# Performance work log

Hardware: AMD Instinct MI355X
Metric: run time of the kernel (lower is better)

Reference implementation:

```python
import jax, jax.numpy as jnp
import numpy as np

V = 23
EDGES = [(2,1),(3,1),(6,12),(6,10),(6,8),(8,10),(7,13),(7,11),(7,9),(9,11),(2,4),(4,6),(3,5),(5,7),(2,3),(2,14),(3,15),(14,15),(14,16),(15,17),(16,18),(17,19),(18,20),(18,22),(20,22),(19,21),(19,23),(21,23)]
K, H, C, OUT_C = 3, 8, 128, 128
N, T = 32, 256
BN_EPS = 1e-5


def _hop_matrix():
    # binarized union of I, Fw, Bw as in Graph.get_hop_distance
    A = np.zeros((V, V))
    for i, j in EDGES:
        A[i - 1, j - 1] = 1.0
        A[j - 1, i - 1] = 1.0
    np.fill_diagonal(A, 1.0)
    hop = np.full((V, V), V, dtype=np.int32)
    P = np.eye(V)
    for d in range(V):
        reach = P > 0
        hop = np.where(reach & (hop == V), d, hop)  # smallest d with reachability
        P = P @ A
    assert hop.max() < V, 'graph must be connected'
    return hop


def setup_inputs() -> dict:
    key = jax.random.key(0)
    ks = jax.random.split(key, 8)
    hop = _hop_matrix()  # (V,V) int32, max hop = 8 for mediapipe layout
    n_hop = int(hop.max()) + 1
    cin_g = C // H            # 16 in-channels per group
    cout_g = OUT_C // H       # 16 out-channels per group
    return {
        'x': jax.random.normal(ks[0], (N, C, T, V), dtype=jnp.float32),
        'emb_table': jax.random.normal(ks[1], (K, H, n_hop), dtype=jnp.float32) * 0.1,
        'A': jnp.tile(jnp.eye(V, dtype=jnp.float32)[None, None], (K, H, 1, 1))
             + 0.01 * jax.random.normal(ks[2], (K, H, V, V), dtype=jnp.float32),
        'conv_w': jax.random.normal(ks[3], (K * OUT_C, cin_g), dtype=jnp.float32) * 0.05,
        'conv_b': jax.random.normal(ks[4], (K * OUT_C,), dtype=jnp.float32) * 0.05,
        'bn_gamma': jax.random.uniform(ks[5], (OUT_C,), dtype=jnp.float32, minval=0.5, maxval=1.5),
        'bn_beta': jax.random.normal(ks[6], (OUT_C,), dtype=jnp.float32) * 0.1,
        'bn_mean': jax.random.normal(ks[7], (OUT_C,), dtype=jnp.float32) * 0.1,
        'bn_var': jax.random.uniform(jax.random.fold_in(key, 99), (OUT_C,), dtype=jnp.float32, minval=0.5, maxval=1.5),
        'hop': jnp.asarray(hop),
    }


def reference(x, emb_table, A, conv_w, conv_b, bn_gamma, bn_beta, bn_mean, bn_var, hop):
    n, c, t, v = x.shape
    k, h = A.shape[0], A.shape[1]
    cin_g = c // h
    # per-kernel/per-head learned adjacency from hop embedding table
    B = emb_table[:, :, hop]                                   # (k,h,v,v)
    def l2(w):
        return jnp.sqrt(jnp.sum(w * w, axis=-2, keepdims=True)) + 1e-4
    BnA = B / l2(B) + A / l2(A)                                # (k,h,v,v)
    xh = x.reshape(n, h, cin_g, t, v)
    # graph mixing over nodes (k-dim broadcast of x)
    y = jnp.einsum('nhctv,khvw->nkhctw', xh, BnA)              # (n,k,h,c/h,t,v)
    # grouped 1x1 conv (groups = k*h): per (k,h) group 16->16 channel mix
    w = conv_w.reshape(k, h, -1, cin_g)                        # (k,h,out/h,c/h)
    b = conv_b.reshape(k, h, -1)                               # (k,h,out/h)
    y = jnp.einsum('nkhctv,khoc->nkhotv', y, w) + b[None, :, :, :, None, None]
    y = y.reshape(n, k, -1, t, v).sum(axis=1)                  # (n,out_c,t,v)
    # BatchNorm2d (eval mode)
    inv = bn_gamma / jnp.sqrt(bn_var + BN_EPS)
    y = y * inv[None, :, None, None] + (bn_beta - bn_mean * inv)[None, :, None, None]
    # residual is identity (in_channels == out_channels)
    return jax.nn.relu(y + x)
```

## Files before the change

### kernel.cpp

```cpp
#include <hip/hip_runtime.h>
#include <hip/hip_bf16.h>
#include <stdint.h>

#define V 23
#define VP 24
#define KK 3
#define H 8
#define CG 16
#define TDIM 256
#define NB 32
#define TT 64
#define OUTC 128
#define CIN 128
#define KDIM 384
#define NSTEP 12
#define NCT 24
#define XROW 392

#define WS_BNA   0
#define WS_SCALE (KK*H*VP*VP)
#define WS_OFFS  (WS_SCALE + OUTC)
#define WS_WT    (WS_OFFS + OUTC)
#define WS_MB    (WS_WT + KK*H*CG*CG)
#define MB_ELEMS ((size_t)H * NSTEP * NCT * 512)
#define WS_NEED_BYTES ((size_t)WS_MB * 4 + MB_ELEMS * 2)
#define WS_SMALL_BYTES ((size_t)WS_MB * 4)

typedef __attribute__((ext_vector_type(8))) short bf16x8;
typedef __attribute__((ext_vector_type(4))) float f32x4;

static __device__ __forceinline__ uint32_t f2bf_rne(float f) {
  uint32_t u = __float_as_uint(f);
  return (u + 0x7fffu + ((u >> 16) & 1u)) >> 16;
}
static __device__ __forceinline__ float bf2f(uint16_t h) {
  return __uint_as_float(((uint32_t)h) << 16);
}

__global__ void prep1_kernel(const float* __restrict__ emb,
                             const float* __restrict__ A,
                             const float* __restrict__ conv_w,
                             const float* __restrict__ conv_b,
                             const float* __restrict__ gamma,
                             const float* __restrict__ beta,
                             const float* __restrict__ mean,
                             const float* __restrict__ var,
                             const int* __restrict__ hop,
                             int n_hop, float* __restrict__ ws) {
  int b = blockIdx.x;
  int tid = threadIdx.x;
  if (b < KK * H) {
    int w = tid;
    if (w >= 32) return;
    const float* e = emb + b * n_hop;
    const float* a = A + b * V * V;
    float nb = 1.f, na = 1.f;
    if (w < V) {
      float sb = 0.f, sa = 0.f;
      for (int v = 0; v < V; ++v) {
        float bv = e[hop[v * V + w]];
        float av = a[v * V + w];
        sb += bv * bv;
        sa += av * av;
      }
      nb = sqrtf(sb) + 1e-4f;
      na = sqrtf(sa) + 1e-4f;
    }
    float* dst = ws + WS_BNA + b * VP * VP;
    if (w < VP) {
      for (int v = 0; v < VP; ++v) {
        float val = 0.f;
        if (v < V && w < V)
          val = e[hop[v * V + w]] / nb + a[v * V + w] / na;
        dst[v * VP + w] = val;
      }
    }
  } else if (b == KK * H) {
    if (tid < OUTC) {
      float inv = gamma[tid] * rsqrtf(var[tid] + 1e-5f);
      float sb = conv_b[tid] + conv_b[OUTC + tid] + conv_b[2 * OUTC + tid];
      ws[WS_SCALE + tid] = inv;
      ws[WS_OFFS + tid] = beta[tid] - mean[tid] * inv + sb * inv;
    }
  } else {
    int idx = (b - KK * H - 1) * 256 + tid;
    if (idx < KK * H * CG * CG) {
      int o = idx & 15, c = (idx >> 4) & 15, h = (idx >> 8) & 7, k = idx >> 11;
      ws[WS_WT + ((k * H + h) * CG + c) * CG + o] =
          conv_w[((k * OUTC) + h * CG + o) * CG + c];
    }
  }
}

__global__ void prep2_kernel(float* __restrict__ ws) {
  int b = blockIdx.x;
  int h = b / NSTEP, s = b % NSTEP;
  uint16_t* mb = (uint16_t*)(ws + WS_MB);
  const float* wt = ws + WS_WT;
  const float* bna = ws + WS_BNA;
  for (int e = threadIdx.x; e < NCT * 64 * 8; e += 256) {
    int j = e & 7, lane = (e >> 3) & 63, ct = e >> 9;
    int k = s * 32 + ((lane >> 4) << 3) + j;
    int ci = k / VP, v = k % VP;
    int col = ct * 16 + (lane & 15);
    int o = col / VP, w = col - o * VP;
    float val = 0.f;
    if (v < V && w < V) {
      for (int kk = 0; kk < KK; ++kk)
        val += wt[((kk * H + h) * CG + ci) * CG + o] *
               bna[((kk * H + h) * VP + v) * VP + w];
    }
    mb[((size_t)(h * NSTEP + s) * NCT + ct) * 512 + lane * 8 + j] =
        (uint16_t)f2bf_rne(val);
  }
}

__global__ __launch_bounds__(256, 3) void gcn_main_mfma(
    const float* __restrict__ x,
    const float* __restrict__ ws,
    float* __restrict__ out) {
  __shared__ __align__(16) uint16_t Xa[TT * XROW];

  const int tid = threadIdx.x;
  const int t0 = blockIdx.x * TT;
  const int h  = blockIdx.y;
  const int n  = blockIdx.z;

  for (int u = tid; u < CG * TT * 6; u += 256) {
    int c = u / (TT * 6);
    int r = u % (TT * 6);
    int tt = r / 6, vc = r % 6;
    const float* xrow =
        x + ((size_t)((n * CIN + h * CG + c) * TDIM) + (t0 + tt)) * V;
    float f0 = xrow[vc * 4 + 0];
    float f1 = xrow[vc * 4 + 1];
    float f2 = xrow[vc * 4 + 2];
    float f3 = (vc < 5) ? xrow[vc * 4 + 3] : 0.f;
    uint32_t lo = f2bf_rne(f0) | (f2bf_rne(f1) << 16);
    uint32_t hi = f2bf_rne(f2) | (f2bf_rne(f3) << 16);
    *(uint2*)&Xa[tt * XROW + c * VP + vc * 4] = make_uint2(lo, hi);
  }
  __syncthreads();

  const int wave = tid >> 6, lane = tid & 63;
  const int m = lane & 15, q = lane >> 4;

  const uint16_t* mb = (const uint16_t*)(ws + WS_MB) +
                       ((size_t)h * NSTEP * NCT + wave * 6) * 512 + lane * 8;

  f32x4 acc[4][6];
#pragma unroll
  for (int rt = 0; rt < 4; ++rt)
#pragma unroll
    for (int c6 = 0; c6 < 6; ++c6) acc[rt][c6] = (f32x4){0.f, 0.f, 0.f, 0.f};

  for (int s = 0; s < NSTEP; ++s) {
    bf16x8 bf[6];
#pragma unroll
    for (int c6 = 0; c6 < 6; ++c6)
      bf[c6] = *(const bf16x8*)(mb + (size_t)(s * NCT + c6) * 512);
    bf16x8 af[4];
#pragma unroll
    for (int rt = 0; rt < 4; ++rt)
      af[rt] = *(const bf16x8*)&Xa[(rt * 16 + m) * XROW + s * 32 + q * 8];
#pragma unroll
    for (int c6 = 0; c6 < 6; ++c6)
#pragma unroll
      for (int rt = 0; rt < 4; ++rt)
        acc[rt][c6] = __builtin_amdgcn_mfma_f32_16x16x32_bf16(
            af[rt], bf[c6], acc[rt][c6], 0, 0, 0);
  }

#pragma unroll
  for (int c6 = 0; c6 < 6; ++c6) {
    int col = (wave * 6 + c6) * 16 + m;
    int o = col / VP, w = col - o * VP;
    float sc = ws[WS_SCALE + h * CG + o];
    float of = ws[WS_OFFS + h * CG + o];
    bool valid = (w < V);
    float* obase =
        out + ((size_t)(n * OUTC + h * CG + o) * TDIM + t0) * V + w;
#pragma unroll
    for (int rt = 0; rt < 4; ++rt) {
#pragma unroll
      for (int reg = 0; reg < 4; ++reg) {
        int row = rt * 16 + q * 4 + reg;
        float resid = bf2f(Xa[row * XROW + col]);
        float y = fmaf(acc[rt][c6][reg], sc, of) + resid;
        if (valid) obase[(size_t)row * V] = fmaxf(y, 0.f);
      }
    }
  }
}

__global__ __launch_bounds__(256, 3) void gcn_main_valu(
    const float* __restrict__ x,
    const float* __restrict__ ws,
    float* __restrict__ out) {
  __shared__ __align__(16) uint16_t Xs[CG * TT * VP];

  const int tid = threadIdx.x;
  const int t0 = blockIdx.x * TT;
  const int h  = blockIdx.y;
  const int n  = blockIdx.z;

  for (int u = tid; u < CG * TT * 6; u += 256) {
    int c = u / (TT * 6);
    int r = u % (TT * 6);
    int tt = r / 6, vc = r % 6;
    const float* xrow =
        x + ((size_t)((n * CIN + h * CG + c) * TDIM) + (t0 + tt)) * V;
    float f0 = xrow[vc * 4 + 0];
    float f1 = xrow[vc * 4 + 1];
    float f2 = xrow[vc * 4 + 2];
    float f3 = (vc < 5) ? xrow[vc * 4 + 3] : 0.f;
    uint32_t lo = f2bf_rne(f0) | (f2bf_rne(f1) << 16);
    uint32_t hi = f2bf_rne(f2) | (f2bf_rne(f3) << 16);
    *(uint2*)&Xs[(c * TT + tt) * VP + vc * 4] = make_uint2(lo, hi);
  }
  __syncthreads();

  const int oq = __builtin_amdgcn_readfirstlane(tid >> 6);
  const int tt = tid & 63;

  const float* wt  = ws + WS_WT  + ((size_t)h * CG * CG);
  const float* bna = ws + WS_BNA + ((size_t)h * VP * VP);

  float acc[4][VP];
#pragma unroll
  for (int o = 0; o < 4; ++o)
#pragma unroll
    for (int w = 0; w < VP; ++w) acc[o][w] = 0.f;

  for (int k = 0; k < KK; ++k) {
    const float* wtk  = wt  + (size_t)k * H * CG * CG;
    const float* bnak = bna + (size_t)k * H * VP * VP;
    for (int vb = 0; vb < 3; ++vb) {
      float xwv[4][8];
#pragma unroll
      for (int o = 0; o < 4; ++o)
#pragma unroll
        for (int j = 0; j < 8; ++j) xwv[o][j] = 0.f;
#pragma unroll 4
      for (int c = 0; c < CG; ++c) {
        uint4 raw = *(const uint4*)&Xs[(c * TT + tt) * VP + vb * 8];
        float4 wv = *(const float4*)&wtk[c * CG + (oq << 2)];
        float xv[8];
        xv[0] = __uint_as_float(raw.x << 16);
        xv[1] = __uint_as_float(raw.x & 0xffff0000u);
        xv[2] = __uint_as_float(raw.y << 16);
        xv[3] = __uint_as_float(raw.y & 0xffff0000u);
        xv[4] = __uint_as_float(raw.z << 16);
        xv[5] = __uint_as_float(raw.z & 0xffff0000u);
        xv[6] = __uint_as_float(raw.w << 16);
        xv[7] = __uint_as_float(raw.w & 0xffff0000u);
#pragma unroll
        for (int o = 0; o < 4; ++o) {
          float wo = (&wv.x)[o];
#pragma unroll
          for (int j = 0; j < 8; ++j) xwv[o][j] = fmaf(wo, xv[j], xwv[o][j]);
        }
      }
#pragma unroll
      for (int j = 0; j < 8; ++j) {
        const int v = vb * 8 + j;
        const float* bnrow = &bnak[v * VP];
#pragma unroll
        for (int wb = 0; wb < 6; ++wb) {
          float4 bn = *(const float4*)(bnrow + wb * 4);
#pragma unroll
          for (int o = 0; o < 4; ++o) {
            acc[o][wb * 4 + 0] = fmaf(xwv[o][j], bn.x, acc[o][wb * 4 + 0]);
            acc[o][wb * 4 + 1] = fmaf(xwv[o][j], bn.y, acc[o][wb * 4 + 1]);
            acc[o][wb * 4 + 2] = fmaf(xwv[o][j], bn.z, acc[o][wb * 4 + 2]);
            acc[o][wb * 4 + 3] = fmaf(xwv[o][j], bn.w, acc[o][wb * 4 + 3]);
          }
        }
      }
    }
  }

#pragma unroll
  for (int o = 0; o < 4; ++o) {
    int og = (oq << 2) + o;
    int oc = h * CG + og;
    float sc = ws[WS_SCALE + oc];
    float of = ws[WS_OFFS + oc];
    float* orow = out + ((size_t)(n * OUTC + oc) * TDIM + (t0 + tt)) * V;
    const uint16_t* xsrow = &Xs[(og * TT + tt) * VP];
#pragma unroll
    for (int w = 0; w < V; ++w) {
      float resid = bf2f(xsrow[w]);
      float y = fmaf(acc[o][w], sc, of) + resid;
      orow[w] = fmaxf(y, 0.f);
    }
  }
}

extern "C" void kernel_launch(void* const* d_in, const int* in_sizes, int n_in,
                              void* d_out, int out_size, void* d_ws, size_t ws_size,
                              hipStream_t stream) {
  const float* x      = (const float*)d_in[0];
  const float* emb    = (const float*)d_in[1];
  const float* A      = (const float*)d_in[2];
  const float* conv_w = (const float*)d_in[3];
  const float* conv_b = (const float*)d_in[4];
  const float* gamma  = (const float*)d_in[5];
  const float* beta   = (const float*)d_in[6];
  const float* mean   = (const float*)d_in[7];
  const float* var    = (const float*)d_in[8];
  const int*   hop    = (const int*)d_in[9];
  float* ws  = (float*)d_ws;
  float* out = (float*)d_out;

  int n_hop = in_sizes[1] / (KK * H);

  prep1_kernel<<<dim3(KK * H + 1 + 24), dim3(256), 0, stream>>>(
      emb, A, conv_w, conv_b, gamma, beta, mean, var, hop, n_hop, ws);

  if (ws_size >= WS_NEED_BYTES) {
    prep2_kernel<<<dim3(H * NSTEP), dim3(256), 0, stream>>>(ws);
    gcn_main_mfma<<<dim3(TDIM / TT, H, NB), dim3(256), 0, stream>>>(x, ws, out);
  } else {
    gcn_main_valu<<<dim3(TDIM / TT, H, NB), dim3(256), 0, stream>>>(x, ws, out);
  }
}
```

Before: 247.6 us.

## Stage MFMA epilogue output through LDS for coalesced stores and batch input loads

The input staging loop now issues all 24 of each thread's global loads into registers before converting to bf16 and writing to shared memory, so more loads are in flight at once. The epilogue computes scale/offset, residual and ReLU, packs the results as bf16, and writes them into the shared buffer in the output's (o, t, v) order. It then streams that buffer out with contiguous, coalesced global stores instead of the previous writes strided by V. The outputs are now rounded to bf16 before being stored as fp32, which lowers output precision. The change also adds two extra block barriers and extra register pressure from the staged loads.

```diff
diff --git a/kernel.cpp b/kernel.cpp
--- a/kernel.cpp
+++ b/kernel.cpp
@@ -24,7 +24,6 @@
 #define WS_MB    (WS_WT + KK*H*CG*CG)
 #define MB_ELEMS ((size_t)H * NSTEP * NCT * 512)
 #define WS_NEED_BYTES ((size_t)WS_MB * 4 + MB_ELEMS * 2)
-#define WS_SMALL_BYTES ((size_t)WS_MB * 4)
 
 typedef __attribute__((ext_vector_type(8))) short bf16x8;
 typedef __attribute__((ext_vector_type(4))) float f32x4;
@@ -126,18 +125,28 @@
   const int h  = blockIdx.y;
   const int n  = blockIdx.z;
 
-  for (int u = tid; u < CG * TT * 6; u += 256) {
+  float xf[24][4];
+#pragma unroll
+  for (int i = 0; i < 24; ++i) {
+    int u = tid + i * 256;
     int c = u / (TT * 6);
     int r = u % (TT * 6);
     int tt = r / 6, vc = r % 6;
     const float* xrow =
         x + ((size_t)((n * CIN + h * CG + c) * TDIM) + (t0 + tt)) * V;
-    float f0 = xrow[vc * 4 + 0];
-    float f1 = xrow[vc * 4 + 1];
-    float f2 = xrow[vc * 4 + 2];
-    float f3 = (vc < 5) ? xrow[vc * 4 + 3] : 0.f;
-    uint32_t lo = f2bf_rne(f0) | (f2bf_rne(f1) << 16);
-    uint32_t hi = f2bf_rne(f2) | (f2bf_rne(f3) << 16);
+    xf[i][0] = xrow[vc * 4 + 0];
+    xf[i][1] = xrow[vc * 4 + 1];
+    xf[i][2] = xrow[vc * 4 + 2];
+    xf[i][3] = (vc < 5) ? xrow[vc * 4 + 3] : 0.f;
+  }
+#pragma unroll
+  for (int i = 0; i < 24; ++i) {
+    int u = tid + i * 256;
+    int c = u / (TT * 6);
+    int r = u % (TT * 6);
+    int tt = r / 6, vc = r % 6;
+    uint32_t lo = f2bf_rne(xf[i][0]) | (f2bf_rne(xf[i][1]) << 16);
+    uint32_t hi = f2bf_rne(xf[i][2]) | (f2bf_rne(xf[i][3]) << 16);
     *(uint2*)&Xa[tt * XROW + c * VP + vc * 4] = make_uint2(lo, hi);
   }
   __syncthreads();
@@ -171,24 +180,58 @@
             af[rt], bf[c6], acc[rt][c6], 0, 0, 0);
   }
 
+  uint32_t pk[6][4][2];
+#pragma unroll
+  for (int c6 = 0; c6 < 6; ++c6) {
+    int col = (wave * 6 + c6) * 16 + m;
+    int o = col / VP;
+    float sc = ws[WS_SCALE + h * CG + o];
+    float of = ws[WS_OFFS + h * CG + o];
+#pragma unroll
+    for (int rt = 0; rt < 4; ++rt) {
+#pragma unroll
+      for (int rg = 0; rg < 2; ++rg) {
+        int row0 = rt * 16 + q * 4 + rg * 2;
+        float y0 = fmaxf(
+            fmaf(acc[rt][c6][rg * 2], sc, of) + bf2f(Xa[row0 * XROW + col]),
+            0.f);
+        float y1 = fmaxf(
+            fmaf(acc[rt][c6][rg * 2 + 1], sc, of) +
+                bf2f(Xa[(row0 + 1) * XROW + col]),
+            0.f);
+        pk[c6][rt][rg] = f2bf_rne(y0) | (f2bf_rne(y1) << 16);
+      }
+    }
+  }
+  __syncthreads();
+
 #pragma unroll
   for (int c6 = 0; c6 < 6; ++c6) {
     int col = (wave * 6 + c6) * 16 + m;
     int o = col / VP, w = col - o * VP;
-    float sc = ws[WS_SCALE + h * CG + o];
-    float of = ws[WS_OFFS + h * CG + o];
-    bool valid = (w < V);
-    float* obase =
-        out + ((size_t)(n * OUTC + h * CG + o) * TDIM + t0) * V + w;
-#pragma unroll
-    for (int rt = 0; rt < 4; ++rt) {
-#pragma unroll
-      for (int reg = 0; reg < 4; ++reg) {
-        int row = rt * 16 + q * 4 + reg;
-        float resid = bf2f(Xa[row * XROW + col]);
-        float y = fmaf(acc[rt][c6][reg], sc, of) + resid;
-        if (valid) obase[(size_t)row * V] = fmaxf(y, 0.f);
-      }
+    if (w < V) {
+#pragma unroll
+      for (int rt = 0; rt < 4; ++rt) {
+#pragma unroll
+        for (int rg = 0; rg < 2; ++rg) {
+          int row = rt * 16 + q * 4 + rg * 2;
+          Xa[(o * TT + row) * V + w] = (uint16_t)(pk[c6][rt][rg] & 0xffffu);
+          Xa[(o * TT + row + 1) * V + w] = (uint16_t)(pk[c6][rt][rg] >> 16);
+        }
+      }
+    }
+  }
+  __syncthreads();
+
+  {
+    const size_t obase0 = ((size_t)(n * OUTC + h * CG) * TDIM + t0) * V;
+    int og = 0, r = tid;
+#pragma unroll 4
+    for (int it = 0; it < 92; ++it) {
+      float val = bf2f(Xa[og * (TT * V) + r]);
+      out[obase0 + (size_t)og * (TDIM * V) + r] = val;
+      r += 256;
+      if (r >= TT * V) { r -= TT * V; ++og; }
     }
   }
 }
```

After: 277.6 us. +12.1%, slower.
